# Kernel optimization log

Measured on AMD Instinct MI355X. Metric: run time of the kernel, lower is better.

Reference implementation:

```python
import jax, jax.numpy as jnp
import numpy as np

B, S, L, H, VIN, VOUT = 64, 64, 64, 256, 10000, 10000


def setup_inputs() -> dict:
    key = jax.random.key(0)
    ks = jax.random.split(key, 14)
    f = lambda k, shp: jax.random.normal(k, shp, dtype=jnp.float32) * 0.05
    return {
        "X": f(ks[0], (B, S, VIN)),
        "ground_truth": jax.random.randint(ks[1], (B, L), 0, VOUT, dtype=jnp.int32),
        "enc_Wih": f(ks[2], (3 * H, VIN)),
        "enc_Whh": f(ks[3], (3 * H, H)),
        "enc_bih": f(ks[4], (3 * H,)),
        "enc_bhh": f(ks[5], (3 * H,)),
        "att_w": f(ks[6], (2 * H,)),
        "att_b": f(ks[7], ()),
        "dec_Wih": f(ks[8], (3 * H, H + VOUT)),
        "dec_Whh": f(ks[9], (3 * H, H)),
        "dec_bih": f(ks[10], (3 * H,)),
        "dec_bhh": f(ks[11], (3 * H,)),
        "out_W": f(ks[12], (VOUT, H)),
        "out_b": f(ks[13], (VOUT,)),
    }


def gru_cell(h, x, Wih, Whh, bih, bhh):
    # PyTorch GRU cell: gates ordered (r, z, n)
    gi = x @ Wih.T + bih          # [B, 3H]
    gh = h @ Whh.T + bhh          # [B, 3H]
    ir, iz, inn = jnp.split(gi, 3, axis=-1)
    hr, hz, hn = jnp.split(gh, 3, axis=-1)
    r = jax.nn.sigmoid(ir + hr)
    z = jax.nn.sigmoid(iz + hz)
    n = jnp.tanh(inn + r * hn)
    return (1.0 - z) * n + z * h


def reference(X, ground_truth, enc_Wih, enc_Whh, enc_bih, enc_bhh,
              att_w, att_b, dec_Wih, dec_Whh, dec_bih, dec_bhh, out_W, out_b):
    b = X.shape[0]
    h_dim = enc_Whh.shape[1]
    vout = out_W.shape[0]

    # ---- encoder GRU over time (time-major scan) ----
    Xs = jnp.transpose(X, (1, 0, 2))                      # [S, B, VIN]
    h0 = jnp.zeros((b, h_dim), X.dtype)

    def enc_step(h, x):
        h2 = gru_cell(h, x, enc_Wih, enc_Whh, enc_bih, enc_bhh)
        return h2, h2

    h_last, enc_h = jax.lax.scan(enc_step, h0, Xs)        # enc_h: [S, B, H]

    # additive attention: logits = relu(W_a [h_dec; enc_h] + b_a)
    w_dec, w_enc = jnp.split(att_w, 2)                    # each [H]
    enc_score = jnp.einsum('sbh,h->sb', enc_h, w_enc)     # precomputed, [S, B]

    gtT = ground_truth.T                                  # [L, B]
    prev0 = jnp.zeros((b, vout), X.dtype)                 # initial one-hot input (zeros)

    def dec_step(carry, gt_i):
        h, prev = carry
        logits = jax.nn.relu(enc_score + h @ w_dec + att_b)   # [S, B]
        wts = jax.nn.softmax(logits, axis=0)                  # softmax over enc positions
        ctx = jnp.einsum('sb,sbh->bh', wts, enc_h)            # [B, H]
        dec_in = jnp.concatenate([ctx, prev], axis=-1)        # [B, H + VOUT]
        h2 = gru_cell(h, dec_in, dec_Wih, dec_Whh, dec_bih, dec_bhh)
        logp = jax.nn.log_softmax(h2 @ out_W.T + out_b, axis=-1)  # [B, VOUT]
        onehot = jax.nn.one_hot(gt_i, vout, dtype=X.dtype)        # teacher forcing
        return (h2, onehot), logp

    _, outs = jax.lax.scan(dec_step, (h_last, prev0), gtT)    # [L, B, VOUT]
    return jnp.transpose(outs, (1, 0, 2))                     # [B, L, VOUT]
```

## Files before the change

kernel.cpp:

```cpp
#include <hip/hip_runtime.h>
#include <hip/hip_bf16.h>
#include <math.h>

#define NB 64
#define NS 64
#define NL 64
#define NH 256
#define G3 768
#define NVIN 10000
#define NVOUT 10000
#define KP2 10240
#define NOUTP 10112

typedef __attribute__((ext_vector_type(8))) short bf16x8;
typedef __attribute__((ext_vector_type(4))) float f32x4;
typedef __attribute__((ext_vector_type(4))) unsigned int u32x4;

__device__ __forceinline__ void gld_lds16(const __hip_bfloat16* g, __hip_bfloat16* l) {
  __builtin_amdgcn_global_load_lds(
      (const __attribute__((address_space(1))) unsigned int*)(const void*)g,
      (__attribute__((address_space(3))) unsigned int*)(void*)l, 16, 0, 0);
}

__device__ __forceinline__ unsigned int f2bf(float f) {
  unsigned int u = __float_as_uint(f);
  return (u + 0x7fff + ((u >> 16) & 1)) >> 16;
}

__device__ __forceinline__ float fast_tanh(float x) {
  float e = __expf(-2.f * x);
  return (1.f - e) / (1.f + e);
}

__device__ __forceinline__ void lds_barrier() {
  asm volatile("s_waitcnt lgkmcnt(0)\n\ts_barrier" ::: "memory");
}

__global__ __launch_bounds__(256) void k_cvt_pad(
    const float* __restrict__ in, __hip_bfloat16* __restrict__ out,
    int in_rows, int in_cols, int out_cols, int swz) {
  int r = blockIdx.x;
  const float* src = in + (size_t)r * in_cols;
  __hip_bfloat16* dst = out + (size_t)r * out_cols;
  bool live = r < in_rows;
  int sx = swz ? ((r & 7) << 3) : 0;
  for (int c = threadIdx.x * 4; c < out_cols; c += 1024) {
    int cc = (c & ~63) | ((c & 63) ^ sx);
    __hip_bfloat16 v[4];
    if (live && cc + 3 < in_cols) {
      float4 f = *(const float4*)(src + cc);
      v[0] = __float2bfloat16(f.x); v[1] = __float2bfloat16(f.y);
      v[2] = __float2bfloat16(f.z); v[3] = __float2bfloat16(f.w);
    } else {
      v[0] = v[1] = v[2] = v[3] = __float2bfloat16(0.f);
    }
    *(ushort4*)(dst + c) = *(const ushort4*)v;
  }
}

__global__ __launch_bounds__(256) void k_wpack(
    const float* __restrict__ srcA, int strideA,
    const float* __restrict__ srcB, int strideB,
    __hip_bfloat16* __restrict__ out, int total) {
  int idx = blockIdx.x * 256 + threadIdx.x;
  if (idx >= total) return;
  int k = idx & 255, c = (idx >> 8) & 255, f = idx >> 16;
  float v = (f < 3) ? srcA[(size_t)(f * 256 + c) * strideA + k]
                    : srcB[(size_t)((f - 3) * 256 + c) * strideB + k];
  out[idx] = __float2bfloat16(v);
}

__global__ __launch_bounds__(256) void k_gemm_encS(
    const __hip_bfloat16* __restrict__ A, const __hip_bfloat16* __restrict__ B,
    float* __restrict__ P) {
  __shared__ __hip_bfloat16 As[128][64];
  __shared__ __hip_bfloat16 Bs[128][64];
  int t = threadIdx.x;
  int wid = t >> 6, lane = t & 63;
  int m0 = blockIdx.y * 128, n0 = blockIdx.x * 128;
  int wr = wid >> 1, wc = wid & 1;
  int r16 = lane & 15, hi16 = lane >> 4;
  int xr = (r16 & 7) << 4;
  f32x4 acc[4][4] = {};
  int kbeg = blockIdx.z * 2560;
  for (int ks = 0; ks < 40; ++ks) {
    int k0 = kbeg + ks * 64;
    __syncthreads();
#pragma unroll
    for (int is = 0; is < 4; ++is) {
      int off = is * 4096 + t * 16;
      int r = off >> 7, e = (off & 127) >> 1;
      gld_lds16(A + (size_t)(m0 + r) * KP2 + k0 + e, &As[r][e]);
      gld_lds16(B + (size_t)(n0 + r) * KP2 + k0 + e, &Bs[r][e]);
    }
    __syncthreads();
    const char* ab = (const char*)As;
    const char* bb = (const char*)Bs;
#pragma unroll
    for (int kk = 0; kk < 2; ++kk) {
      int ko = kk * 64 + hi16 * 16;
      bf16x8 af[4], bfr[4];
#pragma unroll
      for (int i = 0; i < 4; ++i) {
        af[i]  = *(const bf16x8*)(ab + (wr * 64 + i * 16 + r16) * 128 + (ko ^ xr));
        bfr[i] = *(const bf16x8*)(bb + (wc * 64 + i * 16 + r16) * 128 + (ko ^ xr));
      }
#pragma unroll
      for (int i = 0; i < 4; ++i)
#pragma unroll
        for (int j = 0; j < 4; ++j)
          acc[i][j] = __builtin_amdgcn_mfma_f32_16x16x32_bf16(af[i], bfr[j], acc[i][j], 0, 0, 0);
    }
  }
  float* Pz = P + (size_t)blockIdx.z * 4096 * G3;
#pragma unroll
  for (int i = 0; i < 4; ++i)
#pragma unroll
    for (int j = 0; j < 4; ++j) {
      int ccol = n0 + wc * 64 + j * 16 + r16;
#pragma unroll
      for (int q = 0; q < 4; ++q) {
        int crow = m0 + wr * 64 + i * 16 + hi16 * 4 + q;
        Pz[(size_t)crow * G3 + ccol] = acc[i][j][q];
      }
    }
}

__global__ __launch_bounds__(256) void k_reduce4(
    const float4* __restrict__ P, const float* __restrict__ bias,
    float4* __restrict__ G) {
  int idx = blockIdx.x * 256 + threadIdx.x;
  float4 a = P[idx], b = P[idx + 786432], c = P[idx + 2 * 786432],
         d = P[idx + 3 * 786432];
  float4 bs = *(const float4*)(bias + (idx % 192) * 4);
  float4 o;
  o.x = a.x + b.x + c.x + d.x + bs.x;
  o.y = a.y + b.y + c.y + d.y + bs.y;
  o.z = a.z + b.z + c.z + d.z + bs.z;
  o.w = a.w + b.w + c.w + d.w + bs.w;
  G[idx] = o;
}

__global__ __launch_bounds__(256) void k_gemm_outS(
    const __hip_bfloat16* __restrict__ A, const __hip_bfloat16* __restrict__ B,
    const float* __restrict__ bias, float* __restrict__ C) {
  __shared__ __hip_bfloat16 As[128][64];
  __shared__ __hip_bfloat16 Bs[128][64];
  int t = threadIdx.x;
  int wid = t >> 6, lane = t & 63;
  int m0 = blockIdx.y * 128, n0 = blockIdx.x * 128;
  int wr = wid >> 1, wc = wid & 1;
  int r16 = lane & 15, hi16 = lane >> 4;
  int xr = (r16 & 7) << 4;
  f32x4 acc[4][4] = {};
  for (int k0 = 0; k0 < NH; k0 += 64) {
    __syncthreads();
#pragma unroll
    for (int is = 0; is < 4; ++is) {
      int off = is * 4096 + t * 16;
      int r = off >> 7, e = (off & 127) >> 1;
      gld_lds16(A + (size_t)(m0 + r) * NH + k0 + e, &As[r][e]);
      gld_lds16(B + (size_t)(n0 + r) * NH + k0 + e, &Bs[r][e]);
    }
    __syncthreads();
    const char* ab = (const char*)As;
    const char* bb = (const char*)Bs;
#pragma unroll
    for (int kk = 0; kk < 2; ++kk) {
      int ko = kk * 64 + hi16 * 16;
      bf16x8 af[4], bfr[4];
#pragma unroll
      for (int i = 0; i < 4; ++i) {
        af[i]  = *(const bf16x8*)(ab + (wr * 64 + i * 16 + r16) * 128 + (ko ^ xr));
        bfr[i] = *(const bf16x8*)(bb + (wc * 64 + i * 16 + r16) * 128 + (ko ^ xr));
      }
#pragma unroll
      for (int i = 0; i < 4; ++i)
#pragma unroll
        for (int j = 0; j < 4; ++j)
          acc[i][j] = __builtin_amdgcn_mfma_f32_16x16x32_bf16(af[i], bfr[j], acc[i][j], 0, 0, 0);
    }
  }
#pragma unroll
  for (int i = 0; i < 4; ++i)
#pragma unroll
    for (int j = 0; j < 4; ++j) {
      int ccol = n0 + wc * 64 + j * 16 + r16;
      if (ccol < NVOUT) {
        float bs = bias[ccol];
#pragma unroll
        for (int q = 0; q < 4; ++q) {
          int crow = m0 + wr * 64 + i * 16 + hi16 * 4 + q;
          int l = crow >> 6, b = crow & 63;
          C[((size_t)b * NL + l) * NVOUT + ccol] = acc[i][j][q] + bs;
        }
      }
    }
}

__global__ __launch_bounds__(256) void k_gemm_encw(
    const __hip_bfloat16* __restrict__ A, const __hip_bfloat16* __restrict__ B,
    __hip_bfloat16* __restrict__ C) {
  __shared__ __hip_bfloat16 As[128][32];
  __shared__ __hip_bfloat16 Bs[128][32];
  int t = threadIdx.x;
  int wid = t >> 6, lane = t & 63;
  int m0 = blockIdx.y * 128, n0 = blockIdx.x * 128;
  int wr = wid >> 1, wc = wid & 1;
  f32x4 acc[4][4] = {};
  for (int k0 = 0; k0 < NH; k0 += 32) {
    __syncthreads();
#pragma unroll
    for (int is = 0; is < 2; ++is) {
      int off = is * 4096 + wid * 1024 + lane * 16;
      int r = off >> 6, cb = (off & 63) >> 1;
      gld_lds16(A + (size_t)(m0 + r) * NH + k0 + cb, &As[r][cb]);
      gld_lds16(B + (size_t)(n0 + r) * NH + k0 + cb, &Bs[r][cb]);
    }
    __syncthreads();
    int r16 = lane & 15, kb = (lane >> 4) * 8;
    bf16x8 af[4], bfr[4];
#pragma unroll
    for (int i = 0; i < 4; ++i) {
      af[i]  = *(const bf16x8*)&As[wr * 64 + i * 16 + r16][kb];
      bfr[i] = *(const bf16x8*)&Bs[wc * 64 + i * 16 + r16][kb];
    }
#pragma unroll
    for (int i = 0; i < 4; ++i)
#pragma unroll
      for (int j = 0; j < 4; ++j)
        acc[i][j] = __builtin_amdgcn_mfma_f32_16x16x32_bf16(af[i], bfr[j], acc[i][j], 0, 0, 0);
  }
  int r16 = lane & 15, rg = lane >> 4;
#pragma unroll
  for (int i = 0; i < 4; ++i)
#pragma unroll
    for (int j = 0; j < 4; ++j) {
      int ccol = n0 + wc * 64 + j * 16 + r16;
#pragma unroll
      for (int q = 0; q < 4; ++q) {
        int crow = m0 + wr * 64 + i * 16 + rg * 4 + q;
        C[(size_t)crow * G3 + ccol] = __float2bfloat16(acc[i][j][q]);
      }
    }
}

__global__ __launch_bounds__(256) void k_tabs(
    const __hip_bfloat16* __restrict__ ENCW, const float* __restrict__ escoreT,
    __hip_bfloat16* __restrict__ TP, __hip_bfloat16* __restrict__ TQ,
    float* __restrict__ thrG, float* __restrict__ sigG) {
  __shared__ float thrL[64];
  __shared__ int   idxL[64];
  __shared__ float wexpL[64];
  int b = blockIdx.x, t = threadIdx.x;
  if (t < 64) {
    float mine = escoreT[b * 64 + t];
    int rank = 0;
    for (int j = 0; j < 64; ++j) {
      float v = __shfl(mine, j, 64);
      rank += (v > mine) || (v == mine && j < t);
    }
    thrL[rank] = mine;
    idxL[rank] = t;
  }
  __syncthreads();
  if (t < 64) {
    float e = __expf(thrL[t]);
    wexpL[t] = e;
    float s = e;
    for (int off = 1; off < 64; off <<= 1) {
      float o = __shfl_up(s, off, 64);
      if (t >= off) s += o;
    }
    sigG[b * 65 + t + 1] = s;
    if (t == 0) sigG[b * 65] = 0.f;
    thrG[b * 64 + t] = thrL[t];
  }
  __syncthreads();
#pragma unroll
  for (int cc = 0; cc < 3; ++cc) {
    int c = t + cc * 256;
    const __hip_bfloat16* ep = ENCW + (size_t)b * 64 * G3 + c;
    float T = 0.f;
    for (int s = 0; s < 64; ++s) T += __bfloat162float(ep[(size_t)s * G3]);
    float P = 0.f, U = 0.f;
    __hip_bfloat16* tp = TP + (size_t)b * 65 * G3 + c;
    __hip_bfloat16* tq = TQ + (size_t)b * 65 * G3 + c;
    tp[0] = __float2bfloat16(0.f);
    tq[0] = __float2bfloat16(T);
    for (int m = 1; m <= 64; ++m) {
      int j = idxL[m - 1];
      float e = __bfloat162float(ep[(size_t)j * G3]);
      P += wexpL[m - 1] * e;
      U += e;
      tp[(size_t)m * G3] = __float2bfloat16(P);
      tq[(size_t)m * G3] = __float2bfloat16(T - U);
    }
  }
}

__global__ __launch_bounds__(256) void k_pregather(
    const float* __restrict__ Wih, const float* __restrict__ bih,
    const int* __restrict__ gt, float* __restrict__ Gdec) {
  int ib = blockIdx.x;
  int i = ib >> 6, b = ib & 63;
  int tok = (i > 0) ? gt[b * NL + (i - 1)] : -1;
  for (int g = threadIdx.x; g < G3; g += 256) {
    float v = bih[g];
    if (tok >= 0) v += Wih[(size_t)g * (NH + NVOUT) + NH + tok];
    Gdec[(size_t)ib * G3 + g] = v;
  }
}

__global__ __launch_bounds__(512) void k_encoder5(
    const float* __restrict__ Gi, const __hip_bfloat16* __restrict__ Wcat,
    const float* __restrict__ bhh, __hip_bfloat16* __restrict__ enchB) {
  __shared__ __hip_bfloat16 hbf[2][256];
  int t = threadIdx.x, w = t >> 6, lane = t & 63;
  int b = blockIdx.x;
  int r16 = lane & 15, hi16 = lane >> 4;
  int cw = w * 32;
  bf16x8 wv[3][2][8];
#pragma unroll
  for (int f = 0; f < 3; ++f)
#pragma unroll
    for (int fc = 0; fc < 2; ++fc)
#pragma unroll
      for (int kf = 0; kf < 8; ++kf)
        wv[f][fc][kf] = *(const bf16x8*)(Wcat +
            (((size_t)f * 256 + cw + fc * 16 + r16) * 256 + kf * 32 + hi16 * 8));
  float bh0[2], bh1[2], bh2[2];
#pragma unroll
  for (int fc = 0; fc < 2; ++fc) {
    bh0[fc] = bhh[cw + fc * 16 + r16];
    bh1[fc] = bhh[256 + cw + fc * 16 + r16];
    bh2[fc] = bhh[512 + cw + fc * 16 + r16];
  }
  if (t < 256) {
    hbf[0][t] = __float2bfloat16(0.f);
    hbf[1][t] = __float2bfloat16(0.f);
  }
  __syncthreads();
  float hp[2] = {0.f, 0.f};
  int cur = 0;
  for (int s = 0; s < NS; ++s) {
    float gd0[2], gd1[2], gd2[2];
    if (hi16 == 0) {
      const float* gp = Gi + ((size_t)b * 64 + s) * G3;
#pragma unroll
      for (int fc = 0; fc < 2; ++fc) {
        gd0[fc] = gp[cw + fc * 16 + r16];
        gd1[fc] = gp[256 + cw + fc * 16 + r16];
        gd2[fc] = gp[512 + cw + fc * 16 + r16];
      }
    }
    const char* hb = (const char*)&hbf[cur][0];
    f32x4 acc[3][2] = {};
#pragma unroll
    for (int half = 0; half < 2; ++half) {
      bf16x8 ah[4];
#pragma unroll
      for (int kf = 0; kf < 4; ++kf)
        ah[kf] = *(const bf16x8*)(hb + (half * 4 + kf) * 64 + hi16 * 16);
#pragma unroll
      for (int f = 0; f < 3; ++f)
#pragma unroll
        for (int fc = 0; fc < 2; ++fc)
#pragma unroll
          for (int kf = 0; kf < 4; ++kf)
            acc[f][fc] = __builtin_amdgcn_mfma_f32_16x16x32_bf16(
                ah[kf], wv[f][fc][half * 4 + kf], acc[f][fc], 0, 0, 0);
    }
    if (hi16 == 0) {
      int nxt = cur ^ 1;
#pragma unroll
      for (int fc = 0; fc < 2; ++fc) {
        int c = cw + fc * 16 + r16;
        float rr = 1.f / (1.f + __expf(-(gd0[fc] + acc[0][fc][0] + bh0[fc])));
        float zz = 1.f / (1.f + __expf(-(gd1[fc] + acc[1][fc][0] + bh1[fc])));
        float nn = fast_tanh(gd2[fc] + rr * (acc[2][fc][0] + bh2[fc]));
        float hn = (1.f - zz) * nn + zz * hp[fc];
        hp[fc] = hn;
        hbf[nxt][c] = __float2bfloat16(hn);
        enchB[((size_t)b * 64 + s) * 256 + c] = __float2bfloat16(hn);
      }
    }
    lds_barrier();
    cur ^= 1;
  }
}

__global__ __launch_bounds__(256) void k_escoreB(
    const __hip_bfloat16* __restrict__ enchB, const float* __restrict__ att_w,
    float* __restrict__ escoreT) {
  int row = blockIdx.x * 4 + (threadIdx.x >> 6);
  int lane = threadIdx.x & 63;
  ushort4 u = *(const ushort4*)(enchB + (size_t)row * 256 + lane * 4);
  const float* we = att_w + 256 + lane * 4;
  float p = __uint_as_float((unsigned)u.x << 16) * we[0]
          + __uint_as_float((unsigned)u.y << 16) * we[1]
          + __uint_as_float((unsigned)u.z << 16) * we[2]
          + __uint_as_float((unsigned)u.w << 16) * we[3];
#pragma unroll
  for (int off = 32; off; off >>= 1) p += __shfl_xor(p, off, 64);
  if (lane == 0) escoreT[row] = p;
}

__global__ __launch_bounds__(512) void k_decoder8(
    const float* __restrict__ Gdec, const __hip_bfloat16* __restrict__ Wcat6,
    const float* __restrict__ bhh, const __hip_bfloat16* __restrict__ enchB,
    const __hip_bfloat16* __restrict__ TP, const __hip_bfloat16* __restrict__ TQ,
    const float* __restrict__ thrG, const float* __restrict__ sigG,
    const float* __restrict__ att_w, const float* __restrict__ att_b,
    __hip_bfloat16* __restrict__ dechb) {
  __shared__ __hip_bfloat16 hbf[2][256];
  __shared__ float psumL[2][8];
  __shared__ float sigL[65];
  int t = threadIdx.x, w = t >> 6, lane = t & 63;
  int b = blockIdx.x;
  int r16 = lane & 15, hi16 = lane >> 4;
  int cw = w * 32;
  bf16x8 wv[3][2][8];
#pragma unroll
  for (int f = 0; f < 3; ++f)
#pragma unroll
    for (int fc = 0; fc < 2; ++fc)
#pragma unroll
      for (int kf = 0; kf < 8; ++kf)
        wv[f][fc][kf] = *(const bf16x8*)(Wcat6 +
            (((size_t)(3 + f) * 256 + cw + fc * 16 + r16) * 256 + kf * 32 + hi16 * 8));
  float wd0 = att_w[cw + r16], wd1 = att_w[cw + 16 + r16];
  float attb = att_b[0];
  float thr = thrG[(size_t)b * 64 + lane];
  if (t < 65) sigL[t] = sigG[(size_t)b * 65 + t];
  float bh0[2], bh1[2], bh2[2];
#pragma unroll
  for (int fc = 0; fc < 2; ++fc) {
    bh0[fc] = bhh[cw + fc * 16 + r16];
    bh1[fc] = bhh[256 + cw + fc * 16 + r16];
    bh2[fc] = bhh[512 + cw + fc * 16 + r16];
  }
  if (t < 256) {
    hbf[0][t] = enchB[((size_t)b * 64 + 63) * 256 + t];
    hbf[1][t] = __float2bfloat16(0.f);
  }
  float hp[2];
  hp[0] = __bfloat162float(enchB[((size_t)b * 64 + 63) * 256 + cw + r16]);
  hp[1] = __bfloat162float(enchB[((size_t)b * 64 + 63) * 256 + cw + 16 + r16]);
  if (hi16 == 0) {
    float pp = hp[0] * wd0 + hp[1] * wd1;
    pp += __shfl_xor(pp, 1, 64); pp += __shfl_xor(pp, 2, 64);
    pp += __shfl_xor(pp, 4, 64); pp += __shfl_xor(pp, 8, 64);
    if (lane == 0) psumL[0][w] = pp;
  }
  __syncthreads();
  const __hip_bfloat16* tpb = TP + (size_t)b * 65 * G3;
  const __hip_bfloat16* tqb = TQ + (size_t)b * 65 * G3;
  int bs3 = (b & 7) << 3;
  int cur = 0;
  for (int i = 0; i < NL; ++i) {
    float gd0[2], gd1[2], gd2[2];
    if (hi16 == 0) {
      const float* gp = Gdec + ((size_t)i * 64 + b) * G3;
#pragma unroll
      for (int fc = 0; fc < 2; ++fc) {
        gd0[fc] = gp[cw + fc * 16 + r16];
        gd1[fc] = gp[256 + cw + fc * 16 + r16];
        gd2[fc] = gp[512 + cw + fc * 16 + r16];
      }
    }
    float4 pa = *(const float4*)&psumL[cur][0];
    float4 pb = *(const float4*)&psumL[cur][4];
    float d = ((pa.x + pa.y) + (pa.z + pa.w)) + ((pb.x + pb.y) + (pb.z + pb.w)) + attb;
    float ed = __expf(d);
    unsigned long long bal = __ballot(thr + d > 0.f);
    int m = __popcll(bal);
    float tp0 = 0.f, tp1 = 0.f, tq0 = 0.f, tq1 = 0.f, sg = 0.f;
    if (hi16 == 0) {
      const __hip_bfloat16* tpr = tpb + (size_t)m * G3 + cw + r16;
      const __hip_bfloat16* tqr = tqb + (size_t)m * G3 + cw + r16;
      tp0 = __bfloat162float(tpr[0]);  tp1 = __bfloat162float(tpr[16]);
      tq0 = __bfloat162float(tqr[0]);  tq1 = __bfloat162float(tqr[16]);
      sg = sigL[m];
    }
    const char* hb = (const char*)&hbf[cur][0];
    bf16x8 ah[8];
#pragma unroll
    for (int kf = 0; kf < 8; ++kf)
      ah[kf] = *(const bf16x8*)(hb + kf * 64 + hi16 * 16);
    f32x4 acch[3][2] = {};
#pragma unroll
    for (int f = 0; f < 3; ++f)
#pragma unroll
      for (int fc = 0; fc < 2; ++fc)
#pragma unroll
        for (int kf = 0; kf < 8; ++kf)
          acch[f][fc] = __builtin_amdgcn_mfma_f32_16x16x32_bf16(
              ah[kf], wv[f][fc][kf], acch[f][fc], 0, 0, 0);
    if (hi16 == 0) {
      float rn = 1.f / (ed * sg + (float)(64 - m));
      float gi0 = (ed * tp0 + tq0) * rn;
      float gi1 = (ed * tp1 + tq1) * rn;
      int nxt = cur ^ 1;
      float hn2[2];
#pragma unroll
      for (int fc = 0; fc < 2; ++fc) {
        int c = cw + fc * 16 + r16;
        float gi = fc ? gi1 : gi0;
        (void)gi;
        (void)c;
      }
      float tpr0[2], tpz0[2], tpn0[2], tqr0[2], tqz0[2], tqn0[2];
#pragma unroll
      for (int fc = 0; fc < 2; ++fc) {
        int c = cw + fc * 16 + r16;
        tpr0[fc] = __bfloat162float(tpb[(size_t)m * G3 + c]);
        tpz0[fc] = __bfloat162float(tpb[(size_t)m * G3 + 256 + c]);
        tpn0[fc] = __bfloat162float(tpb[(size_t)m * G3 + 512 + c]);
        tqr0[fc] = __bfloat162float(tqb[(size_t)m * G3 + c]);
        tqz0[fc] = __bfloat162float(tqb[(size_t)m * G3 + 256 + c]);
        tqn0[fc] = __bfloat162float(tqb[(size_t)m * G3 + 512 + c]);
      }
#pragma unroll
      for (int fc = 0; fc < 2; ++fc) {
        int c = cw + fc * 16 + r16;
        float gir = (ed * tpr0[fc] + tqr0[fc]) * rn;
        float giz = (ed * tpz0[fc] + tqz0[fc]) * rn;
        float gin = (ed * tpn0[fc] + tqn0[fc]) * rn;
        float rr = 1.f / (1.f + __expf(-(gd0[fc] + gir + acch[0][fc][0] + bh0[fc])));
        float zz = 1.f / (1.f + __expf(-(gd1[fc] + giz + acch[1][fc][0] + bh1[fc])));
        float nn = fast_tanh(gd2[fc] + gin + rr * (acch[2][fc][0] + bh2[fc]));
        float hn = (1.f - zz) * nn + zz * hp[fc];
        hp[fc] = hn; hn2[fc] = hn;
        hbf[nxt][c] = __float2bfloat16(hn);
        int cs = (c & ~63) | ((c & 63) ^ bs3);
        dechb[((size_t)i * 64 + b) * 256 + cs] = __float2bfloat16(hn);
      }
      float pp = hn2[0] * wd0 + hn2[1] * wd1;
      pp += __shfl_xor(pp, 1, 64); pp += __shfl_xor(pp, 2, 64);
      pp += __shfl_xor(pp, 4, 64); pp += __shfl_xor(pp, 8, 64);
      if (lane == 0) psumL[cur ^ 1][w] = pp;
    }
    lds_barrier();
    cur ^= 1;
  }
}

__global__ __launch_bounds__(256) void k_logsoftmax(float* __restrict__ out) {
  float* x = out + (size_t)blockIdx.x * NVOUT;
  __shared__ float red[256];
  int t = threadIdx.x;
  float4 v[10];
  float mx = -1e30f;
#pragma unroll
  for (int ii = 0; ii < 10; ++ii) {
    int slot = ii * 256 + t;
    if (slot < 2500) {
      v[ii] = *(const float4*)(x + slot * 4);
      mx = fmaxf(mx, fmaxf(fmaxf(v[ii].x, v[ii].y), fmaxf(v[ii].z, v[ii].w)));
    }
  }
  red[t] = mx; __syncthreads();
  for (int off = 128; off; off >>= 1) {
    if (t < off) red[t] = fmaxf(red[t], red[t + off]);
    __syncthreads();
  }
  mx = red[0]; __syncthreads();
  float sm = 0.f;
#pragma unroll
  for (int ii = 0; ii < 10; ++ii) {
    int slot = ii * 256 + t;
    if (slot < 2500)
      sm += __expf(v[ii].x - mx) + __expf(v[ii].y - mx)
          + __expf(v[ii].z - mx) + __expf(v[ii].w - mx);
  }
  red[t] = sm; __syncthreads();
  for (int off = 128; off; off >>= 1) {
    if (t < off) red[t] += red[t + off];
    __syncthreads();
  }
  float lse = mx + logf(red[0]);
#pragma unroll
  for (int ii = 0; ii < 10; ++ii) {
    int slot = ii * 256 + t;
    if (slot < 2500) {
      float4 o; o.x = v[ii].x - lse; o.y = v[ii].y - lse;
      o.z = v[ii].z - lse; o.w = v[ii].w - lse;
      *(float4*)(x + slot * 4) = o;
    }
  }
}

extern "C" void kernel_launch(void* const* d_in, const int* in_sizes, int n_in,
                              void* d_out, int out_size, void* d_ws, size_t ws_size,
                              hipStream_t stream) {
  const float* X        = (const float*)d_in[0];
  const int*   gt       = (const int*)  d_in[1];
  const float* enc_Wih  = (const float*)d_in[2];
  const float* enc_Whh  = (const float*)d_in[3];
  const float* enc_bih  = (const float*)d_in[4];
  const float* enc_bhh  = (const float*)d_in[5];
  const float* att_w    = (const float*)d_in[6];
  const float* att_b    = (const float*)d_in[7];
  const float* dec_Wih  = (const float*)d_in[8];
  const float* dec_Whh  = (const float*)d_in[9];
  const float* dec_bih  = (const float*)d_in[10];
  const float* dec_bhh  = (const float*)d_in[11];
  const float* out_W    = (const float*)d_in[12];
  const float* out_b    = (const float*)d_in[13];
  float* out = (float*)d_out;

  float* p = (float*)d_ws;
  float* Gienc  = p; p += NS * NB * G3;
  float* Gdec   = p; p += NL * NB * G3;
  float* escoreT = p; p += NB * NS;
  __hip_bfloat16* q = (__hip_bfloat16*)p;
  __hip_bfloat16* enchBb = q; q += (size_t)NB * NS * NH;
  __hip_bfloat16* Wcat_e = q; q += (size_t)3 * 256 * 256;
  __hip_bfloat16* Wcat_d = q; q += (size_t)6 * 256 * 256;
  __hip_bfloat16* Xb     = q; q += (size_t)4096 * KP2;
  __hip_bfloat16* Wencb  = q; q += (size_t)G3 * KP2;
  __hip_bfloat16* Woutb  = q; q += (size_t)NOUTP * NH;
  __hip_bfloat16* dechb  = q; q += (size_t)NL * NB * NH;
  __hip_bfloat16* ENCW   = (__hip_bfloat16*)Gienc;
  __hip_bfloat16* TP  = Xb;
  __hip_bfloat16* TQ  = Xb + (size_t)64 * 65 * G3;
  float* thrG = (float*)(Xb + (size_t)2 * 64 * 65 * G3);
  float* sigG = thrG + 64 * 64;
  float* Pout = (float*)d_out;

  k_cvt_pad<<<4096, 256, 0, stream>>>(X, Xb, 4096, NVIN, KP2, 1);
  k_cvt_pad<<<G3, 256, 0, stream>>>(enc_Wih, Wencb, G3, NVIN, KP2, 1);
  k_cvt_pad<<<NOUTP, 256, 0, stream>>>(out_W, Woutb, NVOUT, NH, NH, 1);
  k_wpack<<<768, 256, 0, stream>>>(enc_Whh, NH, enc_Whh, NH, Wcat_e, 3 * 65536);
  k_wpack<<<1536, 256, 0, stream>>>(dec_Wih, NH + NVOUT, dec_Whh, NH, Wcat_d, 6 * 65536);
  k_pregather<<<NL * NB, 256, 0, stream>>>(dec_Wih, dec_bih, gt, Gdec);

  k_gemm_encS<<<dim3(6, 32, 4), 256, 0, stream>>>(Xb, Wencb, Pout);
  k_reduce4<<<3072, 256, 0, stream>>>((const float4*)Pout, enc_bih, (float4*)Gienc);
  k_encoder5<<<64, 512, 0, stream>>>(Gienc, Wcat_e, enc_bhh, enchBb);
  k_escoreB<<<1024, 256, 0, stream>>>(enchBb, att_w, escoreT);
  k_gemm_encw<<<dim3(6, 32), 256, 0, stream>>>(enchBb, Wcat_d, ENCW);
  k_tabs<<<64, 256, 0, stream>>>(ENCW, escoreT, TP, TQ, thrG, sigG);
  k_decoder8<<<64, 512, 0, stream>>>(Gdec, Wcat_d, dec_bhh, enchBb, TP, TQ,
                                     thrG, sigG, att_w, att_b, dechb);
  k_gemm_outS<<<dim3(79, 32), 256, 0, stream>>>(dechb, Woutb, out_b, out);
  k_logsoftmax<<<NB * NL, 256, 0, stream>>>(out);
}
```

Baseline: 713.9 us.

## Batch four sequences per recurrent block and stream the n-gate weights

```diff
diff --git a/kernel.cpp b/kernel.cpp
--- a/kernel.cpp
+++ b/kernel.cpp
@@ -26,12 +26,13 @@
   unsigned int u = __float_as_uint(f);
   return (u + 0x7fff + ((u >> 16) & 1)) >> 16;
 }
-
+__device__ __forceinline__ float bf2f(unsigned short u) {
+  return __uint_as_float((unsigned)u << 16);
+}
 __device__ __forceinline__ float fast_tanh(float x) {
   float e = __expf(-2.f * x);
   return (1.f - e) / (1.f + e);
 }
-
 __device__ __forceinline__ void lds_barrier() {
   asm volatile("s_waitcnt lgkmcnt(0)\n\ts_barrier" ::: "memory");
 }
@@ -128,16 +129,16 @@
 
 __global__ __launch_bounds__(256) void k_reduce4(
     const float4* __restrict__ P, const float* __restrict__ bias,
-    float4* __restrict__ G) {
+    ushort4* __restrict__ G) {
   int idx = blockIdx.x * 256 + threadIdx.x;
   float4 a = P[idx], b = P[idx + 786432], c = P[idx + 2 * 786432],
          d = P[idx + 3 * 786432];
   float4 bs = *(const float4*)(bias + (idx % 192) * 4);
-  float4 o;
-  o.x = a.x + b.x + c.x + d.x + bs.x;
-  o.y = a.y + b.y + c.y + d.y + bs.y;
-  o.z = a.z + b.z + c.z + d.z + bs.z;
-  o.w = a.w + b.w + c.w + d.w + bs.w;
+  ushort4 o;
+  o.x = (unsigned short)f2bf(a.x + b.x + c.x + d.x + bs.x);
+  o.y = (unsigned short)f2bf(a.y + b.y + c.y + d.y + bs.y);
+  o.z = (unsigned short)f2bf(a.z + b.z + c.z + d.z + bs.z);
+  o.w = (unsigned short)f2bf(a.w + b.w + c.w + d.w + bs.w);
   G[idx] = o;
 }
 
@@ -301,28 +302,28 @@
 
 __global__ __launch_bounds__(256) void k_pregather(
     const float* __restrict__ Wih, const float* __restrict__ bih,
-    const int* __restrict__ gt, float* __restrict__ Gdec) {
+    const int* __restrict__ gt, __hip_bfloat16* __restrict__ Gdec) {
   int ib = blockIdx.x;
   int i = ib >> 6, b = ib & 63;
   int tok = (i > 0) ? gt[b * NL + (i - 1)] : -1;
   for (int g = threadIdx.x; g < G3; g += 256) {
     float v = bih[g];
     if (tok >= 0) v += Wih[(size_t)g * (NH + NVOUT) + NH + tok];
-    Gdec[(size_t)ib * G3 + g] = v;
-  }
-}
-
-__global__ __launch_bounds__(512) void k_encoder5(
-    const float* __restrict__ Gi, const __hip_bfloat16* __restrict__ Wcat,
+    Gdec[(size_t)ib * G3 + g] = __float2bfloat16(v);
+  }
+}
+
+__global__ __launch_bounds__(512) void k_encoder6(
+    const __hip_bfloat16* __restrict__ Gi, const __hip_bfloat16* __restrict__ Wcat,
     const float* __restrict__ bhh, __hip_bfloat16* __restrict__ enchB) {
-  __shared__ __hip_bfloat16 hbf[2][256];
+  __shared__ __hip_bfloat16 hbf[2][16][256];
   int t = threadIdx.x, w = t >> 6, lane = t & 63;
-  int b = blockIdx.x;
+  int b0 = blockIdx.x * 4;
   int r16 = lane & 15, hi16 = lane >> 4;
   int cw = w * 32;
-  bf16x8 wv[3][2][8];
-#pragma unroll
-  for (int f = 0; f < 3; ++f)
+  bf16x8 wv[2][2][8];
+#pragma unroll
+  for (int f = 0; f < 2; ++f)
 #pragma unroll
     for (int fc = 0; fc < 2; ++fc)
 #pragma unroll
@@ -336,54 +337,67 @@
     bh1[fc] = bhh[256 + cw + fc * 16 + r16];
     bh2[fc] = bhh[512 + cw + fc * 16 + r16];
   }
-  if (t < 256) {
-    hbf[0][t] = __float2bfloat16(0.f);
-    hbf[1][t] = __float2bfloat16(0.f);
+  if (t < 512) {
+    ((unsigned*)&hbf[0][0][0])[t] = 0u;
+    ((unsigned*)&hbf[1][0][0])[t] = 0u;
   }
   __syncthreads();
-  float hp[2] = {0.f, 0.f};
+  float hp[4][2] = {};
+  unsigned long long wna = (unsigned long long)(Wcat + (size_t)2 * 65536);
   int cur = 0;
   for (int s = 0; s < NS; ++s) {
-    float gd0[2], gd1[2], gd2[2];
+    asm volatile("" : "+v"(wna));
+    const __hip_bfloat16* wnp = (const __hip_bfloat16*)wna;
+    unsigned short gg[4][2][3];
     if (hi16 == 0) {
-      const float* gp = Gi + ((size_t)b * 64 + s) * G3;
-#pragma unroll
-      for (int fc = 0; fc < 2; ++fc) {
-        gd0[fc] = gp[cw + fc * 16 + r16];
-        gd1[fc] = gp[256 + cw + fc * 16 + r16];
-        gd2[fc] = gp[512 + cw + fc * 16 + r16];
-      }
-    }
-    const char* hb = (const char*)&hbf[cur][0];
-    f32x4 acc[3][2] = {};
-#pragma unroll
-    for (int half = 0; half < 2; ++half) {
-      bf16x8 ah[4];
-#pragma unroll
-      for (int kf = 0; kf < 4; ++kf)
-        ah[kf] = *(const bf16x8*)(hb + (half * 4 + kf) * 64 + hi16 * 16);
-#pragma unroll
-      for (int f = 0; f < 3; ++f)
-#pragma unroll
-        for (int fc = 0; fc < 2; ++fc)
-#pragma unroll
-          for (int kf = 0; kf < 4; ++kf)
-            acc[f][fc] = __builtin_amdgcn_mfma_f32_16x16x32_bf16(
-                ah[kf], wv[f][fc][half * 4 + kf], acc[f][fc], 0, 0, 0);
+#pragma unroll
+      for (int q = 0; q < 4; ++q) {
+        const unsigned short* gp = (const unsigned short*)
+            (Gi + ((size_t)(b0 + q) * 64 + s) * G3);
+#pragma unroll
+        for (int fc = 0; fc < 2; ++fc) {
+          int c = cw + fc * 16 + lane;
+          gg[q][fc][0] = gp[c]; gg[q][fc][1] = gp[256 + c]; gg[q][fc][2] = gp[512 + c];
+        }
+      }
+    }
+    const char* hb = (const char*)&hbf[cur][0][0];
+    bf16x8 ah[8];
+#pragma unroll
+    for (int kf = 0; kf < 8; ++kf)
+      ah[kf] = *(const bf16x8*)(hb + r16 * 512 + (((kf * 64 + hi16 * 16)) ^ ((r16 & 7) << 4)));
+    f32x4 acc[2][2] = {};
+    f32x4 ghn[2] = {};
+#pragma unroll
+    for (int fc = 0; fc < 2; ++fc) {
+      bf16x8 wn[8];
+#pragma unroll
+      for (int kf = 0; kf < 8; ++kf)
+        wn[kf] = *(const bf16x8*)(wnp +
+            ((size_t)(cw + fc * 16 + r16) * 256 + kf * 32 + hi16 * 8));
+#pragma unroll
+      for (int kf = 0; kf < 8; ++kf) {
+        acc[0][fc] = __builtin_amdgcn_mfma_f32_16x16x32_bf16(ah[kf], wv[0][fc][kf], acc[0][fc], 0, 0, 0);
+        acc[1][fc] = __builtin_amdgcn_mfma_f32_16x16x32_bf16(ah[kf], wv[1][fc][kf], acc[1][fc], 0, 0, 0);
+        ghn[fc]    = __builtin_amdgcn_mfma_f32_16x16x32_bf16(ah[kf], wn[kf], ghn[fc], 0, 0, 0);
+      }
     }
     if (hi16 == 0) {
       int nxt = cur ^ 1;
-#pragma unroll
-      for (int fc = 0; fc < 2; ++fc) {
-        int c = cw + fc * 16 + r16;
-        float rr = 1.f / (1.f + __expf(-(gd0[fc] + acc[0][fc][0] + bh0[fc])));
-        float zz = 1.f / (1.f + __expf(-(gd1[fc] + acc[1][fc][0] + bh1[fc])));
-        float nn = fast_tanh(gd2[fc] + rr * (acc[2][fc][0] + bh2[fc]));
-        float hn = (1.f - zz) * nn + zz * hp[fc];
-        hp[fc] = hn;
-        hbf[nxt][c] = __float2bfloat16(hn);
-        enchB[((size_t)b * 64 + s) * 256 + c] = __float2bfloat16(hn);
-      }
+      char* hw = (char*)&hbf[nxt][0][0];
+#pragma unroll
+      for (int q = 0; q < 4; ++q)
+#pragma unroll
+        for (int fc = 0; fc < 2; ++fc) {
+          int c = cw + fc * 16 + lane;
+          float rr = 1.f / (1.f + __expf(-(bf2f(gg[q][fc][0]) + acc[0][fc][q] + bh0[fc])));
+          float zz = 1.f / (1.f + __expf(-(bf2f(gg[q][fc][1]) + acc[1][fc][q] + bh1[fc])));
+          float nn = fast_tanh(bf2f(gg[q][fc][2]) + rr * (ghn[fc][q] + bh2[fc]));
+          float hn = (1.f - zz) * nn + zz * hp[q][fc];
+          hp[q][fc] = hn;
+          *(unsigned short*)(hw + q * 512 + ((2 * c) ^ (q << 4))) = (unsigned short)f2bf(hn);
+          enchB[((size_t)(b0 + q) * 64 + s) * 256 + c] = __float2bfloat16(hn);
+        }
     }
     lds_barrier();
     cur ^= 1;
@@ -397,42 +411,43 @@
   int lane = threadIdx.x & 63;
   ushort4 u = *(const ushort4*)(enchB + (size_t)row * 256 + lane * 4);
   const float* we = att_w + 256 + lane * 4;
-  float p = __uint_as_float((unsigned)u.x << 16) * we[0]
-          + __uint_as_float((unsigned)u.y << 16) * we[1]
-          + __uint_as_float((unsigned)u.z << 16) * we[2]
-          + __uint_as_float((unsigned)u.w << 16) * we[3];
+  float p = bf2f(u.x) * we[0] + bf2f(u.y) * we[1]
+          + bf2f(u.z) * we[2] + bf2f(u.w) * we[3];
 #pragma unroll
   for (int off = 32; off; off >>= 1) p += __shfl_xor(p, off, 64);
   if (lane == 0) escoreT[row] = p;
 }
 
-__global__ __launch_bounds__(512) void k_decoder8(
-    const float* __restrict__ Gdec, const __hip_bfloat16* __restrict__ Wcat6,
+__global__ __launch_bounds__(512) void k_decoder9(
+    const __hip_bfloat16* __restrict__ Gdec, const __hip_bfloat16* __restrict__ Wcat6,
     const float* __restrict__ bhh, const __hip_bfloat16* __restrict__ enchB,
     const __hip_bfloat16* __restrict__ TP, const __hip_bfloat16* __restrict__ TQ,
     const float* __restrict__ thrG, const float* __restrict__ sigG,
     const float* __restrict__ att_w, const float* __restrict__ att_b,
     __hip_bfloat16* __restrict__ dechb) {
-  __shared__ __hip_bfloat16 hbf[2][256];
-  __shared__ float psumL[2][8];
-  __shared__ float sigL[65];
+  __shared__ __hip_bfloat16 hbf[2][16][256];
+  __shared__ float psumL[2][8][4];
+  __shared__ float sigL[4][65];
   int t = threadIdx.x, w = t >> 6, lane = t & 63;
-  int b = blockIdx.x;
+  int b0 = blockIdx.x * 4;
   int r16 = lane & 15, hi16 = lane >> 4;
   int cw = w * 32;
-  bf16x8 wv[3][2][8];
-#pragma unroll
-  for (int f = 0; f < 3; ++f)
+  bf16x8 wv[2][2][8];
+#pragma unroll
+  for (int f = 0; f < 2; ++f)
 #pragma unroll
     for (int fc = 0; fc < 2; ++fc)
 #pragma unroll
       for (int kf = 0; kf < 8; ++kf)
         wv[f][fc][kf] = *(const bf16x8*)(Wcat6 +
             (((size_t)(3 + f) * 256 + cw + fc * 16 + r16) * 256 + kf * 32 + hi16 * 8));
-  float wd0 = att_w[cw + r16], wd1 = att_w[cw + 16 + r16];
+  float wd[2];
+  wd[0] = att_w[cw + r16]; wd[1] = att_w[cw + 16 + r16];
   float attb = att_b[0];
-  float thr = thrG[(size_t)b * 64 + lane];
-  if (t < 65) sigL[t] = sigG[(size_t)b * 65 + t];
+  float thrq[4];
+#pragma unroll
+  for (int q = 0; q < 4; ++q) thrq[q] = thrG[(size_t)(b0 + q) * 64 + lane];
+  if (t < 260) sigL[t / 65][t % 65] = sigG[(size_t)(b0 + t / 65) * 65 + t % 65];
   float bh0[2], bh1[2], bh2[2];
 #pragma unroll
   for (int fc = 0; fc < 2; ++fc) {
@@ -440,106 +455,129 @@
     bh1[fc] = bhh[256 + cw + fc * 16 + r16];
     bh2[fc] = bhh[512 + cw + fc * 16 + r16];
   }
-  if (t < 256) {
-    hbf[0][t] = enchB[((size_t)b * 64 + 63) * 256 + t];
-    hbf[1][t] = __float2bfloat16(0.f);
-  }
-  float hp[2];
-  hp[0] = __bfloat162float(enchB[((size_t)b * 64 + 63) * 256 + cw + r16]);
-  hp[1] = __bfloat162float(enchB[((size_t)b * 64 + 63) * 256 + cw + 16 + r16]);
+  if (t < 1024) {
+    int q = t >> 8, c = t & 255;
+    unsigned short v = ((const unsigned short*)enchB)[((size_t)(b0 + q) * 64 + 63) * 256 + c];
+    *(unsigned short*)((char*)&hbf[0][0][0] + q * 512 + ((2 * c) ^ (q << 4))) = v;
+  }
+  float hp[4][2];
   if (hi16 == 0) {
-    float pp = hp[0] * wd0 + hp[1] * wd1;
-    pp += __shfl_xor(pp, 1, 64); pp += __shfl_xor(pp, 2, 64);
-    pp += __shfl_xor(pp, 4, 64); pp += __shfl_xor(pp, 8, 64);
-    if (lane == 0) psumL[0][w] = pp;
+#pragma unroll
+    for (int q = 0; q < 4; ++q) {
+      const unsigned short* hq = (const unsigned short*)enchB + ((size_t)(b0 + q) * 64 + 63) * 256;
+      hp[q][0] = bf2f(hq[cw + lane]);
+      hp[q][1] = bf2f(hq[cw + 16 + lane]);
+    }
+    float pp[4];
+#pragma unroll
+    for (int q = 0; q < 4; ++q) pp[q] = hp[q][0] * wd[0] + hp[q][1] * wd[1];
+#pragma unroll
+    for (int off = 1; off < 16; off <<= 1)
+#pragma unroll
+      for (int q = 0; q < 4; ++q) pp[q] += __shfl_xor(pp[q], off, 64);
+    if (lane == 0) { float4 v4 = {pp[0], pp[1], pp[2], pp[3]}; *(float4*)&psumL[0][w][0] = v4; }
   }
   __syncthreads();
-  const __hip_bfloat16* tpb = TP + (size_t)b * 65 * G3;
-  const __hip_bfloat16* tqb = TQ + (size_t)b * 65 * G3;
-  int bs3 = (b & 7) << 3;
+  unsigned long long wna = (unsigned long long)(Wcat6 + (size_t)5 * 65536);
   int cur = 0;
   for (int i = 0; i < NL; ++i) {
-    float gd0[2], gd1[2], gd2[2];
+    asm volatile("" : "+v"(wna));
+    const __hip_bfloat16* wnp = (const __hip_bfloat16*)wna;
+    unsigned short gg[4][2][3];
     if (hi16 == 0) {
-      const float* gp = Gdec + ((size_t)i * 64 + b) * G3;
-#pragma unroll
-      for (int fc = 0; fc < 2; ++fc) {
-        gd0[fc] = gp[cw + fc * 16 + r16];
-        gd1[fc] = gp[256 + cw + fc * 16 + r16];
-        gd2[fc] = gp[512 + cw + fc * 16 + r16];
-      }
-    }
-    float4 pa = *(const float4*)&psumL[cur][0];
-    float4 pb = *(const float4*)&psumL[cur][4];
-    float d = ((pa.x + pa.y) + (pa.z + pa.w)) + ((pb.x + pb.y) + (pb.z + pb.w)) + attb;
-    float ed = __expf(d);
-    unsigned long long bal = __ballot(thr + d > 0.f);
-    int m = __popcll(bal);
-    float tp0 = 0.f, tp1 = 0.f, tq0 = 0.f, tq1 = 0.f, sg = 0.f;
+#pragma unroll
+      for (int q = 0; q < 4; ++q) {
+        const unsigned short* gp = (const unsigned short*)
+            (Gdec + ((size_t)i * 64 + b0 + q) * G3);
+#pragma unroll
+        for (int fc = 0; fc < 2; ++fc) {
+          int c = cw + fc * 16 + lane;
+          gg[q][fc][0] = gp[c]; gg[q][fc][1] = gp[256 + c]; gg[q][fc][2] = gp[512 + c];
+        }
+      }
+    }
+    float dq[4] = {};
+#pragma unroll
+    for (int wq = 0; wq < 8; ++wq) {
+      float4 v4 = *(const float4*)&psumL[cur][wq][0];
+      dq[0] += v4.x; dq[1] += v4.y; dq[2] += v4.z; dq[3] += v4.w;
+    }
+    float ed[4]; int m[4];
+#pragma unroll
+    for (int q = 0; q < 4; ++q) {
+      dq[q] += attb;
+      ed[q] = __expf(dq[q]);
+      m[q] = __popcll(__ballot(thrq[q] + dq[q] > 0.f));
+    }
+    unsigned short tpv[4][2][3], tqv[4][2][3];
+    float sg[4];
     if (hi16 == 0) {
-      const __hip_bfloat16* tpr = tpb + (size_t)m * G3 + cw + r16;
-      const __hip_bfloat16* tqr = tqb + (size_t)m * G3 + cw + r16;
-      tp0 = __bfloat162float(tpr[0]);  tp1 = __bfloat162float(tpr[16]);
-      tq0 = __bfloat162float(tqr[0]);  tq1 = __bfloat162float(tqr[16]);
-      sg = sigL[m];
-    }
-    const char* hb = (const char*)&hbf[cur][0];
+#pragma unroll
+      for (int q = 0; q < 4; ++q) {
+        const unsigned short* tpr = (const unsigned short*)TP + ((size_t)(b0 + q) * 65 + m[q]) * G3;
+        const unsigned short* tqr = (const unsigned short*)TQ + ((size_t)(b0 + q) * 65 + m[q]) * G3;
+        sg[q] = sigL[q][m[q]];
+#pragma unroll
+        for (int fc = 0; fc < 2; ++fc) {
+          int c = cw + fc * 16 + lane;
+          tpv[q][fc][0] = tpr[c]; tpv[q][fc][1] = tpr[256 + c]; tpv[q][fc][2] = tpr[512 + c];
+          tqv[q][fc][0] = tqr[c]; tqv[q][fc][1] = tqr[256 + c]; tqv[q][fc][2] = tqr[512 + c];
+        }
+      }
+    }
+    const char* hb = (const char*)&hbf[cur][0][0];
     bf16x8 ah[8];
 #pragma unroll
     for (int kf = 0; kf < 8; ++kf)
-      ah[kf] = *(const bf16x8*)(hb + kf * 64 + hi16 * 16);
-    f32x4 acch[3][2] = {};
-#pragma unroll
-    for (int f = 0; f < 3; ++f)
-#pragma unroll
-      for (int fc = 0; fc < 2; ++fc)
-#pragma unroll
-        for (int kf = 0; kf < 8; ++kf)
-          acch[f][fc] = __builtin_amdgcn_mfma_f32_16x16x32_bf16(
-              ah[kf], wv[f][fc][kf], acch[f][fc], 0, 0, 0);
+      ah[kf] = *(const bf16x8*)(hb + r16 * 512 + (((kf * 64 + hi16 * 16)) ^ ((r16 & 7) << 4)));
+    f32x4 acch[2][2] = {};
+    f32x4 ghn[2] = {};
+#pragma unroll
+    for (int fc = 0; fc < 2; ++fc) {
+      bf16x8 wn[8];
+#pragma unroll
+      for (int kf = 0; kf < 8; ++kf)
+        wn[kf] = *(const bf16x8*)(wnp +
+            ((size_t)(cw + fc * 16 + r16) * 256 + kf * 32 + hi16 * 8));
+#pragma unroll
+      for (int kf = 0; kf < 8; ++kf) {
+        acch[0][fc] = __builtin_amdgcn_mfma_f32_16x16x32_bf16(ah[kf], wv[0][fc][kf], acch[0][fc], 0, 0, 0);
+        acch[1][fc] = __builtin_amdgcn_mfma_f32_16x16x32_bf16(ah[kf], wv[1][fc][kf], acch[1][fc], 0, 0, 0);
+        ghn[fc]     = __builtin_amdgcn_mfma_f32_16x16x32_bf16(ah[kf], wn[kf], ghn[fc], 0, 0, 0);
+      }
+    }
     if (hi16 == 0) {
-      float rn = 1.f / (ed * sg + (float)(64 - m));
-      float gi0 = (ed * tp0 + tq0) * rn;
-      float gi1 = (ed * tp1 + tq1) * rn;
       int nxt = cur ^ 1;
-      float hn2[2];
-#pragma unroll
-      for (int fc = 0; fc < 2; ++fc) {
-        int c = cw + fc * 16 + r16;
-        float gi = fc ? gi1 : gi0;
-        (void)gi;
-        (void)c;
-      }
-      float tpr0[2], tpz0[2], tpn0[2], tqr0[2], tqz0[2], tqn0[2];
-#pragma unroll
-      for (int fc = 0; fc < 2; ++fc) {
-        int c = cw + fc * 16 + r16;
-        tpr0[fc] = __bfloat162float(tpb[(size_t)m * G3 + c]);
-        tpz0[fc] = __bfloat162float(tpb[(size_t)m * G3 + 256 + c]);
-        tpn0[fc] = __bfloat162float(tpb[(size_t)m * G3 + 512 + c]);
-        tqr0[fc] = __bfloat162float(tqb[(size_t)m * G3 + c]);
-        tqz0[fc] = __bfloat162float(tqb[(size_t)m * G3 + 256 + c]);
-        tqn0[fc] = __bfloat162float(tqb[(size_t)m * G3 + 512 + c]);
-      }
-#pragma unroll
-      for (int fc = 0; fc < 2; ++fc) {
-        int c = cw + fc * 16 + r16;
-        float gir = (ed * tpr0[fc] + tqr0[fc]) * rn;
-        float giz = (ed * tpz0[fc] + tqz0[fc]) * rn;
-        float gin = (ed * tpn0[fc] + tqn0[fc]) * rn;
-        float rr = 1.f / (1.f + __expf(-(gd0[fc] + gir + acch[0][fc][0] + bh0[fc])));
-        float zz = 1.f / (1.f + __expf(-(gd1[fc] + giz + acch[1][fc][0] + bh1[fc])));
-        float nn = fast_tanh(gd2[fc] + gin + rr * (acch[2][fc][0] + bh2[fc]));
-        float hn = (1.f - zz) * nn + zz * hp[fc];
-        hp[fc] = hn; hn2[fc] = hn;
-        hbf[nxt][c] = __float2bfloat16(hn);
-        int cs = (c & ~63) | ((c & 63) ^ bs3);
-        dechb[((size_t)i * 64 + b) * 256 + cs] = __float2bfloat16(hn);
-      }
-      float pp = hn2[0] * wd0 + hn2[1] * wd1;
-      pp += __shfl_xor(pp, 1, 64); pp += __shfl_xor(pp, 2, 64);
-      pp += __shfl_xor(pp, 4, 64); pp += __shfl_xor(pp, 8, 64);
-      if (lane == 0) psumL[cur ^ 1][w] = pp;
+      char* hw = (char*)&hbf[nxt][0][0];
+      float rn[4];
+#pragma unroll
+      for (int q = 0; q < 4; ++q) rn[q] = 1.f / (ed[q] * sg[q] + (float)(64 - m[q]));
+      float pp[4];
+#pragma unroll
+      for (int q = 0; q < 4; ++q) {
+        float hnf[2];
+#pragma unroll
+        for (int fc = 0; fc < 2; ++fc) {
+          int c = cw + fc * 16 + lane;
+          float gir = (ed[q] * bf2f(tpv[q][fc][0]) + bf2f(tqv[q][fc][0])) * rn[q];
+          float giz = (ed[q] * bf2f(tpv[q][fc][1]) + bf2f(tqv[q][fc][1])) * rn[q];
+          float gin = (ed[q] * bf2f(tpv[q][fc][2]) + bf2f(tqv[q][fc][2])) * rn[q];
+          float rr = 1.f / (1.f + __expf(-(bf2f(gg[q][fc][0]) + gir + acch[0][fc][q] + bh0[fc])));
+          float zz = 1.f / (1.f + __expf(-(bf2f(gg[q][fc][1]) + giz + acch[1][fc][q] + bh1[fc])));
+          float nn = fast_tanh(bf2f(gg[q][fc][2]) + gin + rr * (ghn[fc][q] + bh2[fc]));
+          float hn = (1.f - zz) * nn + zz * hp[q][fc];
+          hp[q][fc] = hn; hnf[fc] = hn;
+          *(unsigned short*)(hw + q * 512 + ((2 * c) ^ (q << 4))) = (unsigned short)f2bf(hn);
+          int cs = (c & ~63) | ((c & 63) ^ (((b0 + q) & 7) << 3));
+          dechb[((size_t)i * 64 + b0 + q) * 256 + cs] = __float2bfloat16(hn);
+        }
+        pp[q] = hnf[0] * wd[0] + hnf[1] * wd[1];
+      }
+#pragma unroll
+      for (int off = 1; off < 16; off <<= 1)
+#pragma unroll
+        for (int q = 0; q < 4; ++q) pp[q] += __shfl_xor(pp[q], off, 64);
+      if (lane == 0) { float4 v4 = {pp[0], pp[1], pp[2], pp[3]}; *(float4*)&psumL[cur ^ 1][w][0] = v4; }
     }
     lds_barrier();
     cur ^= 1;
@@ -622,7 +660,9 @@
   __hip_bfloat16* Wencb  = q; q += (size_t)G3 * KP2;
   __hip_bfloat16* Woutb  = q; q += (size_t)NOUTP * NH;
   __hip_bfloat16* dechb  = q; q += (size_t)NL * NB * NH;
-  __hip_bfloat16* ENCW   = (__hip_bfloat16*)Gienc;
+  __hip_bfloat16* Gienc_b = (__hip_bfloat16*)Gienc;
+  __hip_bfloat16* Gdec_b  = (__hip_bfloat16*)Gdec;
+  __hip_bfloat16* ENCW   = (__hip_bfloat16*)Gienc + (size_t)4096 * G3;
   __hip_bfloat16* TP  = Xb;
   __hip_bfloat16* TQ  = Xb + (size_t)64 * 65 * G3;
   float* thrG = (float*)(Xb + (size_t)2 * 64 * 65 * G3);
@@ -634,15 +674,15 @@
   k_cvt_pad<<<NOUTP, 256, 0, stream>>>(out_W, Woutb, NVOUT, NH, NH, 1);
   k_wpack<<<768, 256, 0, stream>>>(enc_Whh, NH, enc_Whh, NH, Wcat_e, 3 * 65536);
   k_wpack<<<1536, 256, 0, stream>>>(dec_Wih, NH + NVOUT, dec_Whh, NH, Wcat_d, 6 * 65536);
-  k_pregather<<<NL * NB, 256, 0, stream>>>(dec_Wih, dec_bih, gt, Gdec);
+  k_pregather<<<NL * NB, 256, 0, stream>>>(dec_Wih, dec_bih, gt, Gdec_b);
 
   k_gemm_encS<<<dim3(6, 32, 4), 256, 0, stream>>>(Xb, Wencb, Pout);
-  k_reduce4<<<3072, 256, 0, stream>>>((const float4*)Pout, enc_bih, (float4*)Gienc);
-  k_encoder5<<<64, 512, 0, stream>>>(Gienc, Wcat_e, enc_bhh, enchBb);
+  k_reduce4<<<3072, 256, 0, stream>>>((const float4*)Pout, enc_bih, (ushort4*)Gienc_b);
+  k_encoder6<<<16, 512, 0, stream>>>(Gienc_b, Wcat_e, enc_bhh, enchBb);
   k_escoreB<<<1024, 256, 0, stream>>>(enchBb, att_w, escoreT);
   k_gemm_encw<<<dim3(6, 32), 256, 0, stream>>>(enchBb, Wcat_d, ENCW);
   k_tabs<<<64, 256, 0, stream>>>(ENCW, escoreT, TP, TQ, thrG, sigG);
-  k_decoder8<<<64, 512, 0, stream>>>(Gdec, Wcat_d, dec_bhh, enchBb, TP, TQ,
+  k_decoder9<<<16, 512, 0, stream>>>(Gdec_b, Wcat_d, dec_bhh, enchBb, TP, TQ,
                                      thrG, sigG, att_w, att_b, dechb);
   k_gemm_outS<<<dim3(79, 32), 256, 0, stream>>>(dechb, Woutb, out_b, out);
   k_logsoftmax<<<NB * NL, 256, 0, stream>>>(out);
```

New measurement: 1.498 ms. 110% more time.
